# Kernel tuning notes

Hardware: AMD Instinct MI355X
Metric: run time of the kernel (lower is better)

Reference implementation:

```python
import jax, jax.numpy as jnp
import numpy as np


def gcn_conv(h, W, b, src, dst):
    # PyG GCNConv: h @ W, add self-loops, symmetric deg^-1/2 normalization,
    # scatter-add messages from src to dst, then add bias.
    n = h.shape[0]
    h = h @ W                                   # [N, out]
    loop = jnp.arange(n, dtype=src.dtype)
    row = jnp.concatenate([src, loop])          # message sources
    col = jnp.concatenate([dst, loop])          # aggregation targets
    deg = jax.ops.segment_sum(jnp.ones_like(col, dtype=h.dtype), col, num_segments=n)
    dinv = jnp.where(deg > 0, jax.lax.rsqrt(deg), 0.0)
    norm = dinv[row] * dinv[col]                # [E+N]
    out = jax.ops.segment_sum(h[row] * norm[:, None], col, num_segments=n)
    return out + b


def setup_inputs() -> dict:
    key = jax.random.key(0)
    ks = jax.random.split(key, 12)
    N, E = 50000, 800000
    in_dim, hid, out_dim = 768, 256, 128
    x = jax.random.normal(ks[0], (N, in_dim), dtype=jnp.float32)
    edge_index = jax.random.randint(ks[1], (2, E), 0, N, dtype=jnp.int64)

    def lin(k, fan_in, fan_out):
        bound = 1.0 / np.sqrt(fan_in)
        kw, kb = jax.random.split(k)
        W = jax.random.uniform(kw, (fan_in, fan_out), jnp.float32, -bound, bound)
        b = jax.random.uniform(kb, (fan_out,), jnp.float32, -bound, bound)
        return W, b

    W1, b1 = lin(ks[2], in_dim, hid)
    Wg1, bg1 = lin(ks[3], hid, hid)
    Wg2, bg2 = lin(ks[4], hid, hid)
    W2, b2 = lin(ks[5], hid, out_dim)
    Wc, bc = lin(ks[6], out_dim, 2)
    return {
        "x": x, "edge_index": edge_index,
        "W1": W1, "b1": b1, "Wg1": Wg1, "bg1": bg1,
        "Wg2": Wg2, "bg2": bg2, "W2": W2, "b2": b2,
        "Wc": Wc, "bc": bc, "batch_size": 1024,
    }


def reference(x, edge_index, W1, b1, Wg1, bg1, Wg2, bg2, W2, b2, Wc, bc, batch_size):
    src, dst = edge_index[0], edge_index[1]
    h = jax.nn.relu(x @ W1 + b1)                # linear_relu1
    h = gcn_conv(h, Wg1, bg1, src, dst)         # text1
    # dropout is identity in eval mode
    h = gcn_conv(h, Wg2, bg2, src, dst)         # text2
    h = jax.nn.relu(h @ W2 + b2)                # linear_relu2
    logits = h @ Wc + bc                        # classifier
    return logits[:batch_size]
```

## Files before the change

### kernel.cpp

```cpp
#include <hip/hip_runtime.h>
#include <hip/hip_bf16.h>
#include <cstdint>
#include <cstddef>
#include <type_traits>

typedef _Float16 half8 __attribute__((ext_vector_type(8)));
typedef _Float16 half4v __attribute__((ext_vector_type(4)));
typedef float float4v __attribute__((ext_vector_type(4)));


__global__ void k_zero_int(int* __restrict__ p, int n) {
  int i = blockIdx.x * blockDim.x + threadIdx.x;
  if (i < n) p[i] = 0;
}

__global__ void k_count(const int* __restrict__ dst, int* __restrict__ cnt, int E) {
  int e = blockIdx.x * blockDim.x + threadIdx.x;
  if (e < E) atomicAdd(&cnt[dst[e]], 1);
}

__global__ __launch_bounds__(1024) void k_scan_local(const int* __restrict__ cnt,
                                                     int* __restrict__ rowp,
                                                     int* __restrict__ bsum, int n) {
  __shared__ int sm[1024];
  int tid = threadIdx.x;
  int i = blockIdx.x * 1024 + tid;
  int v = (i < n) ? cnt[i] : 0;
  sm[tid] = v;
  __syncthreads();
  for (int off = 1; off < 1024; off <<= 1) {
    int t = (tid >= off) ? sm[tid - off] : 0;
    __syncthreads();
    sm[tid] += t;
    __syncthreads();
  }
  if (i < n) rowp[i] = sm[tid] - v;
  if (tid == 1023) bsum[blockIdx.x] = sm[1023];
}

__global__ __launch_bounds__(1024) void k_scan_sums(int* __restrict__ bsum, int nb) {
  __shared__ int sm[1024];
  int tid = threadIdx.x;
  int v = (tid < nb) ? bsum[tid] : 0;
  sm[tid] = v;
  __syncthreads();
  for (int off = 1; off < 1024; off <<= 1) {
    int t = (tid >= off) ? sm[tid - off] : 0;
    __syncthreads();
    sm[tid] += t;
    __syncthreads();
  }
  if (tid < nb) bsum[tid] = sm[tid] - v;
}

__global__ void k_finalize(int* __restrict__ rowp, const int* __restrict__ bsum,
                           const int* __restrict__ cnt, int* __restrict__ cursor,
                           float* __restrict__ dinv, int n, int E) {
  int i = blockIdx.x * blockDim.x + threadIdx.x;
  if (i < n) {
    int v = rowp[i] + bsum[i >> 10];
    rowp[i] = v;
    cursor[i] = v;
    dinv[i] = rsqrtf((float)(cnt[i] + 1));
  }
  if (i == 0) rowp[n] = E;
}

__global__ void k_fill(const int* __restrict__ src, const int* __restrict__ dst,
                       int* __restrict__ cursor, int* __restrict__ csr_src, int E) {
  int e = blockIdx.x * blockDim.x + threadIdx.x;
  if (e < E) {
    int pos = atomicAdd(&cursor[dst[e]], 1);
    csr_src[pos] = src[e];
  }
}


__global__ void k_w_convert_all(const float* __restrict__ W1, const float* __restrict__ Wg1,
                                const float* __restrict__ Wg2, _Float16* __restrict__ W1t,
                                _Float16* __restrict__ Wg1t, _Float16* __restrict__ Wg2t,
                                int in_dim, int hid) {
  int idx = blockIdx.x * blockDim.x + threadIdx.x;
  int n1 = in_dim * hid;
  int n2 = hid * hid;
  if (idx < n1) {
    int n = idx / in_dim, k = idx - n * in_dim;
    W1t[idx] = (_Float16)W1[(size_t)k * hid + n];
  } else if (idx < n1 + n2) {
    int i2 = idx - n1;
    int n = i2 / hid, k = i2 - n * hid;
    Wg1t[i2] = (_Float16)Wg1[(size_t)k * hid + n];
  } else if (idx < n1 + 2 * n2) {
    int i2 = idx - n1 - n2;
    int n = i2 / hid, k = i2 - n * hid;
    Wg2t[i2] = (_Float16)Wg2[(size_t)k * hid + n];
  }
}


#define LDSS 40

template <typename AT>
__device__ __forceinline__ half8 load_row_h8(const AT* __restrict__ p, bool ok) {
  half8 v = {};
  if (ok) {
    if constexpr (std::is_same_v<AT, float>) {
      float4 f0 = *(const float4*)p;
      float4 f1 = *(const float4*)(p + 4);
      v[0] = (_Float16)f0.x; v[1] = (_Float16)f0.y;
      v[2] = (_Float16)f0.z; v[3] = (_Float16)f0.w;
      v[4] = (_Float16)f1.x; v[5] = (_Float16)f1.y;
      v[6] = (_Float16)f1.z; v[7] = (_Float16)f1.w;
    } else {
      v = *(const half8*)p;
    }
  }
  return v;
}

template <typename AT, int RELU, int BIAS, int SCALE>
__global__ __launch_bounds__(256, 4) void k_gemm_mfma(const AT* __restrict__ A,
                                                      const _Float16* __restrict__ Bt,
                                                      const float* __restrict__ bias,
                                                      const float* __restrict__ rowscale,
                                                      _Float16* __restrict__ out,
                                                      int M, int N, int K) {
  __shared__ _Float16 Asm[2][64 * LDSS];
  __shared__ _Float16 Bsm[2][128 * LDSS];
  const int tid = threadIdx.x;
  const int bm = blockIdx.y * 64;
  const int bn = blockIdx.x * 128;
  const int wave = tid >> 6;
  const int wm = (wave >> 1) * 32;
  const int wn = (wave & 1) * 64;
  const int quad = (tid & 63) >> 4;
  const int l15 = tid & 15;

  const int ar = tid >> 2;
  const int ac = (tid & 3) * 8;
  const int br0 = tid >> 1;

  const int gra = bm + ar;
  const bool oka = gra < M;
  const AT* Apt = A + (size_t)gra * K + ac;
  const int br_0 = tid >> 2, bc_0 = (tid & 3) * 8;
  const int br_1 = (tid + 256) >> 2, bc_1 = ((tid + 256) & 3) * 8;
  const _Float16* Bp0 = Bt + (size_t)(bn + br_0) * K + bc_0;
  const _Float16* Bp1 = Bt + (size_t)(bn + br_1) * K + bc_1;

  _Float16* AsW = &Asm[0][0] + ar * LDSS + ac;
  _Float16* BsW0 = &Bsm[0][0] + br_0 * LDSS + bc_0;
  _Float16* BsW1 = &Bsm[0][0] + br_1 * LDSS + bc_1;
  const int abufstep = 64 * LDSS;
  const int bbufstep = 128 * LDSS;
  (void)br0;

  float4v acc[2][4];
#pragma unroll
  for (int i = 0; i < 2; ++i)
#pragma unroll
    for (int j = 0; j < 4; ++j) acc[i][j] = (float4v){0.f, 0.f, 0.f, 0.f};

  half8 pa = load_row_h8<AT>(Apt, oka);
  half8 pb0 = *(const half8*)Bp0;
  half8 pb1 = *(const half8*)Bp1;
  *(half8*)AsW = pa;
  *(half8*)BsW0 = pb0;
  *(half8*)BsW1 = pb1;

  const int nk = K >> 5;
  int buf = 0;
  for (int kt = 0; kt < nk; ++kt) {
    __syncthreads();
    if (kt + 1 < nk) {
      int k0 = (kt + 1) << 5;
      pa = load_row_h8<AT>(Apt + k0, oka);
      pb0 = *(const half8*)(Bp0 + k0);
      pb1 = *(const half8*)(Bp1 + k0);
    }
    const _Float16* Ab = &Asm[0][0] + buf * abufstep;
    const _Float16* Bb = &Bsm[0][0] + buf * bbufstep;
    half8 af[2], bf[4];
#pragma unroll
    for (int i = 0; i < 2; ++i)
      af[i] = *(const half8*)(Ab + (wm + i * 16 + l15) * LDSS + quad * 8);
#pragma unroll
    for (int j = 0; j < 4; ++j)
      bf[j] = *(const half8*)(Bb + (wn + j * 16 + l15) * LDSS + quad * 8);
#pragma unroll
    for (int i = 0; i < 2; ++i)
#pragma unroll
      for (int j = 0; j < 4; ++j)
        acc[i][j] = __builtin_amdgcn_mfma_f32_16x16x32_f16(af[i], bf[j], acc[i][j], 0, 0, 0);
    if (kt + 1 < nk) {
      int nbuf = buf ^ 1;
      *(half8*)(AsW + nbuf * abufstep) = pa;
      *(half8*)(BsW0 + nbuf * bbufstep) = pb0;
      *(half8*)(BsW1 + nbuf * bbufstep) = pb1;
    }
    buf ^= 1;
  }

#pragma unroll
  for (int j = 0; j < 4; ++j) {
    int c = bn + wn + j * 16 + l15;
    float bv = BIAS ? bias[c] : 0.f;
#pragma unroll
    for (int i = 0; i < 2; ++i) {
      int rbase = bm + wm + i * 16 + quad * 4;
      float4v a = acc[i][j];
#pragma unroll
      for (int reg = 0; reg < 4; ++reg) {
        int r = rbase + reg;
        if (r < M) {
          float v = a[reg] + bv;
          if (RELU) v = fmaxf(v, 0.f);
          if (SCALE) v *= rowscale[r];
          out[(size_t)r * N + c] = (_Float16)v;
        }
      }
    }
  }
}


template <int RELU, int BIAS>
__global__ __launch_bounds__(256) void k_gemm(const float* __restrict__ A,
                                              const float* __restrict__ B,
                                              const float* __restrict__ bias,
                                              float* __restrict__ C,
                                              int M, int N, int K) {
  __shared__ float As[16][68];
  __shared__ float Bs[16][68];
  const int bm = blockIdx.y * 64;
  const int bn = blockIdx.x * 64;
  const int tid = threadIdx.x;
  const int tr = (tid >> 4) << 2;
  const int tc = (tid & 15) << 2;
  const int lm  = tid >> 2;
  const int lk  = (tid & 3) << 2;
  const int lk2 = tid >> 4;
  const int ln  = (tid & 15) << 2;
  const bool arow_ok = (bm + lm) < M;
  const float* Aptr = A + (size_t)(bm + lm) * K + lk;
  const float* Bptr = B + (size_t)lk2 * N + bn + ln;
  float acc[4][4] = {};
  for (int k0 = 0; k0 < K; k0 += 16) {
    float4 a4 = make_float4(0.f, 0.f, 0.f, 0.f);
    if (arow_ok) a4 = *(const float4*)(Aptr + k0);
    float4 b4 = *(const float4*)(Bptr + (size_t)k0 * N);
    As[lk + 0][lm] = a4.x;
    As[lk + 1][lm] = a4.y;
    As[lk + 2][lm] = a4.z;
    As[lk + 3][lm] = a4.w;
    *(float4*)&Bs[lk2][ln] = b4;
    __syncthreads();
#pragma unroll
    for (int k = 0; k < 16; ++k) {
      float4 av = *(const float4*)&As[k][tr];
      float4 bv = *(const float4*)&Bs[k][tc];
      float a[4] = {av.x, av.y, av.z, av.w};
      float b[4] = {bv.x, bv.y, bv.z, bv.w};
#pragma unroll
      for (int i = 0; i < 4; ++i)
#pragma unroll
        for (int j = 0; j < 4; ++j) acc[i][j] += a[i] * b[j];
    }
    __syncthreads();
  }
  float bias_v[4] = {0.f, 0.f, 0.f, 0.f};
  if (BIAS) {
    float4 bb = *(const float4*)(bias + bn + tc);
    bias_v[0] = bb.x; bias_v[1] = bb.y; bias_v[2] = bb.z; bias_v[3] = bb.w;
  }
#pragma unroll
  for (int i = 0; i < 4; ++i) {
    int r = bm + tr + i;
    if (r < M) {
      float4 o;
      o.x = acc[i][0] + bias_v[0];
      o.y = acc[i][1] + bias_v[1];
      o.z = acc[i][2] + bias_v[2];
      o.w = acc[i][3] + bias_v[3];
      if (RELU) {
        o.x = fmaxf(o.x, 0.f); o.y = fmaxf(o.y, 0.f);
        o.z = fmaxf(o.z, 0.f); o.w = fmaxf(o.w, 0.f);
      }
      *(float4*)&C[(size_t)r * N + bn + tc] = o;
    }
  }
}


template <typename OT>
__global__ __launch_bounds__(256) void k_agg(const _Float16* __restrict__ t,
                                             const int* __restrict__ row_ptr,
                                             const int* __restrict__ csr_src,
                                             const float* __restrict__ dinv,
                                             const float* __restrict__ bias,
                                             OT* __restrict__ out, int n_nodes) {
  int w = (int)((blockIdx.x * 256 + threadIdx.x) >> 6);
  int lane = threadIdx.x & 63;
  if (w >= n_nodes) return;
  float di = dinv[w];
  half4v v = *(const half4v*)(t + (size_t)w * 256 + lane * 4);
  float ax = (float)v[0], ay = (float)v[1], az = (float)v[2], aw = (float)v[3];
  int e0 = row_ptr[w], e1 = row_ptr[w + 1];
  int e = e0;
  for (; e + 4 <= e1; e += 4) {
    int s0 = csr_src[e];
    int s1 = csr_src[e + 1];
    int s2 = csr_src[e + 2];
    int s3 = csr_src[e + 3];
    half4v u0 = *(const half4v*)(t + (size_t)s0 * 256 + lane * 4);
    half4v u1 = *(const half4v*)(t + (size_t)s1 * 256 + lane * 4);
    half4v u2 = *(const half4v*)(t + (size_t)s2 * 256 + lane * 4);
    half4v u3 = *(const half4v*)(t + (size_t)s3 * 256 + lane * 4);
    ax += (float)u0[0] + (float)u1[0] + (float)u2[0] + (float)u3[0];
    ay += (float)u0[1] + (float)u1[1] + (float)u2[1] + (float)u3[1];
    az += (float)u0[2] + (float)u1[2] + (float)u2[2] + (float)u3[2];
    aw += (float)u0[3] + (float)u1[3] + (float)u2[3] + (float)u3[3];
  }
  for (; e < e1; ++e) {
    int s = csr_src[e];
    half4v u = *(const half4v*)(t + (size_t)s * 256 + lane * 4);
    ax += (float)u[0]; ay += (float)u[1]; az += (float)u[2]; aw += (float)u[3];
  }
  const float4 b = ((const float4*)bias)[lane];
  if constexpr (std::is_same_v<OT, float>) {
    float4 o;
    o.x = ax * di + b.x; o.y = ay * di + b.y;
    o.z = az * di + b.z; o.w = aw * di + b.w;
    ((float4*)(out + (size_t)w * 256))[lane] = o;
  } else {
    half4v o;
    o[0] = (_Float16)(ax * di + b.x); o[1] = (_Float16)(ay * di + b.y);
    o[2] = (_Float16)(az * di + b.z); o[3] = (_Float16)(aw * di + b.w);
    *(half4v*)(out + (size_t)w * 256 + lane * 4) = o;
  }
}


__global__ __launch_bounds__(256) void k_cls(const float* __restrict__ h,
                                             const float* __restrict__ Wc,
                                             const float* __restrict__ bc,
                                             float* __restrict__ out, int M, int K) {
  __shared__ float w[512];
  for (int i = threadIdx.x; i < 2 * K; i += 256) w[i] = Wc[i];
  __syncthreads();
  int i = blockIdx.x * 256 + threadIdx.x;
  if (i >= M) return;
  float a0 = bc[0], a1 = bc[1];
  const float* hr = h + (size_t)i * K;
  for (int k = 0; k < K; ++k) {
    float a = hr[k];
    a0 += a * w[2 * k];
    a1 += a * w[2 * k + 1];
  }
  out[2 * i] = a0;
  out[2 * i + 1] = a1;
}


extern "C" void kernel_launch(void* const* d_in, const int* in_sizes, int n_in,
                              void* d_out, int out_size, void* d_ws, size_t ws_size,
                              hipStream_t stream) {
  const float* x   = (const float*)d_in[0];
  const int*   ei  = (const int*)d_in[1];
  const float* W1  = (const float*)d_in[2];
  const float* b1  = (const float*)d_in[3];
  const float* Wg1 = (const float*)d_in[4];
  const float* bg1 = (const float*)d_in[5];
  const float* Wg2 = (const float*)d_in[6];
  const float* bg2 = (const float*)d_in[7];
  const float* W2  = (const float*)d_in[8];
  const float* b2  = (const float*)d_in[9];
  const float* Wc  = (const float*)d_in[10];
  const float* bc  = (const float*)d_in[11];
  float* out = (float*)d_out;

  const int hid     = in_sizes[3];
  const int in_dim  = in_sizes[2] / hid;
  const int out_dim = in_sizes[9];
  const int N       = in_sizes[0] / in_dim;
  const int E       = in_sizes[1] / 2;
  const int Batch   = out_size / 2;

  const int* srcI = ei;
  const int* dstI = ei + E;

  char* ws = (char*)d_ws;
  size_t off = 0;
  auto alloc = [&](size_t bytes) -> void* {
    void* p = ws + off;
    off = (off + bytes + 255) & ~(size_t)255;
    return p;
  };
  _Float16* h0h  = (_Float16*)alloc((size_t)N * hid * 2);
  _Float16* t1h  = (_Float16*)alloc((size_t)N * hid * 2);
  _Float16* h1h  = (_Float16*)alloc((size_t)N * hid * 2);
  _Float16* t2h  = (_Float16*)alloc((size_t)N * hid * 2);
  _Float16* W1t  = (_Float16*)alloc((size_t)in_dim * hid * 2);
  _Float16* Wg1t = (_Float16*)alloc((size_t)hid * hid * 2);
  _Float16* Wg2t = (_Float16*)alloc((size_t)hid * hid * 2);
  float* agg2    = (float*)alloc((size_t)Batch * hid * 4);
  float* h3      = (float*)alloc((size_t)Batch * out_dim * 4);
  float* dinv    = (float*)alloc((size_t)N * 4);
  int*   cnt     = (int*)alloc((size_t)N * 4);
  int*   rowp    = (int*)alloc((size_t)(N + 1) * 4);
  int*   bsum    = (int*)alloc((size_t)1024 * 4);
  int*   cursor  = (int*)alloc((size_t)N * 4);
  int*   csrs    = (int*)alloc((size_t)E * 4);
  (void)ws_size; (void)n_in;

  dim3 blk(256);
  const int nb = (N + 1023) / 1024;

  k_zero_int<<<(N + 255) / 256, blk, 0, stream>>>(cnt, N);
  k_count<<<(E + 255) / 256, blk, 0, stream>>>(dstI, cnt, E);
  k_scan_local<<<nb, 1024, 0, stream>>>(cnt, rowp, bsum, N);
  k_scan_sums<<<1, 1024, 0, stream>>>(bsum, nb);
  k_finalize<<<(N + 255) / 256, blk, 0, stream>>>(rowp, bsum, cnt, cursor, dinv, N, E);
  k_fill<<<(E + 255) / 256, blk, 0, stream>>>(srcI, dstI, cursor, csrs, E);

  {
    int total = in_dim * hid + 2 * hid * hid;
    k_w_convert_all<<<(total + 255) / 256, blk, 0, stream>>>(W1, Wg1, Wg2, W1t, Wg1t, Wg2t, in_dim, hid);
  }

  dim3 gemm_grid(hid / 128, (N + 63) / 64);
  k_gemm_mfma<float, 1, 1, 0><<<gemm_grid, blk, 0, stream>>>(x, W1t, b1, nullptr, h0h, N, hid, in_dim);
  k_gemm_mfma<_Float16, 0, 0, 1><<<gemm_grid, blk, 0, stream>>>(h0h, Wg1t, nullptr, dinv, t1h, N, hid, hid);
  k_agg<_Float16><<<(N + 3) / 4, blk, 0, stream>>>(t1h, rowp, csrs, dinv, bg1, h1h, N);
  k_gemm_mfma<_Float16, 0, 0, 1><<<gemm_grid, blk, 0, stream>>>(h1h, Wg2t, nullptr, dinv, t2h, N, hid, hid);
  k_agg<float><<<(Batch + 3) / 4, blk, 0, stream>>>(t2h, rowp, csrs, dinv, bg2, agg2, Batch);
  k_gemm<1, 1><<<dim3(out_dim / 64, (Batch + 63) / 64), blk, 0, stream>>>(agg2, W2, b2, h3, Batch, out_dim, hid);
  k_cls<<<(Batch + 255) / 256, blk, 0, stream>>>(h3, Wc, bc, out, Batch, out_dim);
}
```

Baseline: 534.1 us.

## Use direct global-to-LDS loads, 128x128 tiles and XCD-aware block remap in MFMA GEMM

The MFMA GEMM now loads A and B tiles with global_load_lds, which writes straight into shared memory and skips the register round trip. For the fp32 first layer, A is staged in LDS as fp32 and converted to fp16 when fragments are read. The block tile grows from 64x128 to 128x128, giving each wave 4x4 MFMA accumulators and more reuse. Blocks are launched on a 1D grid and remapped so consecutive tiles land on the same XCD, which should improve L2 locality. In exchange, the padded LDS layout is dropped (possible bank conflicts), register pressure rises (launch bounds lowered to 3), fp32 A tiles double LDS use, and out-of-range rows are clamped rather than zeroed.

```diff
diff --git a/kernel.cpp b/kernel.cpp
--- a/kernel.cpp
+++ b/kernel.cpp
@@ -98,106 +98,125 @@
 }
 
 
-#define LDSS 40
-
-template <typename AT>
-__device__ __forceinline__ half8 load_row_h8(const AT* __restrict__ p, bool ok) {
-  half8 v = {};
-  if (ok) {
-    if constexpr (std::is_same_v<AT, float>) {
-      float4 f0 = *(const float4*)p;
-      float4 f1 = *(const float4*)(p + 4);
-      v[0] = (_Float16)f0.x; v[1] = (_Float16)f0.y;
-      v[2] = (_Float16)f0.z; v[3] = (_Float16)f0.w;
-      v[4] = (_Float16)f1.x; v[5] = (_Float16)f1.y;
-      v[6] = (_Float16)f1.z; v[7] = (_Float16)f1.w;
-    } else {
-      v = *(const half8*)p;
-    }
-  }
-  return v;
+__device__ __forceinline__ void gl_lds16(const void* g, void* l) {
+  __builtin_amdgcn_global_load_lds(
+      (const __attribute__((address_space(1))) void*)g,
+      (__attribute__((address_space(3))) void*)l, 16, 0, 0);
 }
 
 template <typename AT, int RELU, int BIAS, int SCALE>
-__global__ __launch_bounds__(256, 4) void k_gemm_mfma(const AT* __restrict__ A,
+__global__ __launch_bounds__(256, 3) void k_gemm_mfma(const AT* __restrict__ A,
                                                       const _Float16* __restrict__ Bt,
                                                       const float* __restrict__ bias,
                                                       const float* __restrict__ rowscale,
                                                       _Float16* __restrict__ out,
-                                                      int M, int N, int K) {
-  __shared__ _Float16 Asm[2][64 * LDSS];
-  __shared__ _Float16 Bsm[2][128 * LDSS];
+                                                      int M, int N, int K, int gx) {
+  __shared__ alignas(16) AT Asm[2][128 * 32];
+  __shared__ alignas(16) _Float16 Bsm[2][128 * 32];
+  constexpr int RA = (int)sizeof(AT);
+  constexpr int ABUFB = 128 * 32 * (int)sizeof(AT);
+  constexpr int BBUFB = 128 * 32 * 2;
+
   const int tid = threadIdx.x;
-  const int bm = blockIdx.y * 64;
-  const int bn = blockIdx.x * 128;
-  const int wave = tid >> 6;
-  const int wm = (wave >> 1) * 32;
-  const int wn = (wave & 1) * 64;
-  const int quad = (tid & 63) >> 4;
-  const int l15 = tid & 15;
-
-  const int ar = tid >> 2;
-  const int ac = (tid & 3) * 8;
-  const int br0 = tid >> 1;
-
-  const int gra = bm + ar;
-  const bool oka = gra < M;
-  const AT* Apt = A + (size_t)gra * K + ac;
-  const int br_0 = tid >> 2, bc_0 = (tid & 3) * 8;
-  const int br_1 = (tid + 256) >> 2, bc_1 = ((tid + 256) & 3) * 8;
-  const _Float16* Bp0 = Bt + (size_t)(bn + br_0) * K + bc_0;
-  const _Float16* Bp1 = Bt + (size_t)(bn + br_1) * K + bc_1;
-
-  _Float16* AsW = &Asm[0][0] + ar * LDSS + ac;
-  _Float16* BsW0 = &Bsm[0][0] + br_0 * LDSS + bc_0;
-  _Float16* BsW1 = &Bsm[0][0] + br_1 * LDSS + bc_1;
-  const int abufstep = 64 * LDSS;
-  const int bbufstep = 128 * LDSS;
-  (void)br0;
-
-  float4v acc[2][4];
-#pragma unroll
-  for (int i = 0; i < 2; ++i)
+  const int wv = tid >> 6;
+  const int ln = tid & 63;
+  const int quad = ln >> 4;
+  const int l15 = ln & 15;
+  const int wm = (wv >> 1) * 64;
+  const int wn = (wv & 1) * 64;
+
+  const int nwg = (int)gridDim.x;
+  const int orig = (int)blockIdx.x;
+  const int q = nwg >> 3, r = nwg & 7;
+  const int xcd = orig & 7, idx = orig >> 3;
+  const int wg = (xcd < r ? xcd * (q + 1) : r * (q + 1) + (xcd - r) * q) + idx;
+  const int bx = wg % gx;
+  const int by = wg / gx;
+  const int bm = by * 128;
+  const int bn = bx * 128;
+
+  const char* aSrcB[RA];
+  int aDstOff[RA];
+#pragma unroll
+  for (int rr = 0; rr < RA; ++rr) {
+    int p = rr * 4096 + wv * 1024 + ln * 16;
+    int row = p / (32 * (int)sizeof(AT));
+    int colB = p - row * 32 * (int)sizeof(AT);
+    int grow = bm + row; if (grow > M - 1) grow = M - 1;
+    aSrcB[rr] = (const char*)(A + (size_t)grow * K) + colB;
+    aDstOff[rr] = rr * 4096 + wv * 1024;
+  }
+  const char* bSrcB[2];
+  int bDstOff[2];
+#pragma unroll
+  for (int rr = 0; rr < 2; ++rr) {
+    int p = rr * 4096 + wv * 1024 + ln * 16;
+    int row = p >> 6;
+    int colB = p & 63;
+    bSrcB[rr] = (const char*)(Bt + (size_t)(bn + row) * K) + colB;
+    bDstOff[rr] = rr * 4096 + wv * 1024;
+  }
+
+  float4v acc[4][4];
+#pragma unroll
+  for (int i = 0; i < 4; ++i)
 #pragma unroll
     for (int j = 0; j < 4; ++j) acc[i][j] = (float4v){0.f, 0.f, 0.f, 0.f};
 
-  half8 pa = load_row_h8<AT>(Apt, oka);
-  half8 pb0 = *(const half8*)Bp0;
-  half8 pb1 = *(const half8*)Bp1;
-  *(half8*)AsW = pa;
-  *(half8*)BsW0 = pb0;
-  *(half8*)BsW1 = pb1;
-
   const int nk = K >> 5;
+
+  {
+    char* abase = (char*)&Asm[0][0];
+    char* bbase = (char*)&Bsm[0][0];
+#pragma unroll
+    for (int rr = 0; rr < RA; ++rr) gl_lds16(aSrcB[rr], abase + aDstOff[rr]);
+#pragma unroll
+    for (int rr = 0; rr < 2; ++rr) gl_lds16(bSrcB[rr], bbase + bDstOff[rr]);
+  }
+  __syncthreads();
+
   int buf = 0;
   for (int kt = 0; kt < nk; ++kt) {
-    __syncthreads();
     if (kt + 1 < nk) {
-      int k0 = (kt + 1) << 5;
-      pa = load_row_h8<AT>(Apt + k0, oka);
-      pb0 = *(const half8*)(Bp0 + k0);
-      pb1 = *(const half8*)(Bp1 + k0);
+      const size_t advA = (size_t)(kt + 1) * 32 * sizeof(AT);
+      const size_t advB = (size_t)(kt + 1) * 64;
+      char* abase = (char*)&Asm[0][0] + (buf ^ 1) * ABUFB;
+      char* bbase = (char*)&Bsm[0][0] + (buf ^ 1) * BBUFB;
+#pragma unroll
+      for (int rr = 0; rr < RA; ++rr) gl_lds16(aSrcB[rr] + advA, abase + aDstOff[rr]);
+#pragma unroll
+      for (int rr = 0; rr < 2; ++rr) gl_lds16(bSrcB[rr] + advB, bbase + bDstOff[rr]);
     }
-    const _Float16* Ab = &Asm[0][0] + buf * abufstep;
-    const _Float16* Bb = &Bsm[0][0] + buf * bbufstep;
-    half8 af[2], bf[4];
-#pragma unroll
-    for (int i = 0; i < 2; ++i)
-      af[i] = *(const half8*)(Ab + (wm + i * 16 + l15) * LDSS + quad * 8);
+
+    const AT* Ab = &Asm[buf][0];
+    const _Float16* Bb = &Bsm[buf][0];
+    half8 af[4], bf[4];
+#pragma unroll
+    for (int i = 0; i < 4; ++i) {
+      int rowa = wm + i * 16 + l15;
+      if constexpr (std::is_same_v<AT, float>) {
+        float4v f0 = *(const float4v*)(Ab + rowa * 32 + quad * 8);
+        float4v f1 = *(const float4v*)(Ab + rowa * 32 + quad * 8 + 4);
+        half8 h;
+        h[0] = (_Float16)f0[0]; h[1] = (_Float16)f0[1];
+        h[2] = (_Float16)f0[2]; h[3] = (_Float16)f0[3];
+        h[4] = (_Float16)f1[0]; h[5] = (_Float16)f1[1];
+        h[6] = (_Float16)f1[2]; h[7] = (_Float16)f1[3];
+        af[i] = h;
+      } else {
+        af[i] = *(const half8*)(Ab + rowa * 32 + quad * 8);
+      }
+    }
 #pragma unroll
     for (int j = 0; j < 4; ++j)
-      bf[j] = *(const half8*)(Bb + (wn + j * 16 + l15) * LDSS + quad * 8);
-#pragma unroll
-    for (int i = 0; i < 2; ++i)
+      bf[j] = *(const half8*)(Bb + (wn + j * 16 + l15) * 32 + quad * 8);
+#pragma unroll
+    for (int i = 0; i < 4; ++i)
 #pragma unroll
       for (int j = 0; j < 4; ++j)
         acc[i][j] = __builtin_amdgcn_mfma_f32_16x16x32_f16(af[i], bf[j], acc[i][j], 0, 0, 0);
-    if (kt + 1 < nk) {
-      int nbuf = buf ^ 1;
-      *(half8*)(AsW + nbuf * abufstep) = pa;
-      *(half8*)(BsW0 + nbuf * bbufstep) = pb0;
-      *(half8*)(BsW1 + nbuf * bbufstep) = pb1;
-    }
+
+    __syncthreads();
     buf ^= 1;
   }
 
@@ -206,17 +225,17 @@
     int c = bn + wn + j * 16 + l15;
     float bv = BIAS ? bias[c] : 0.f;
 #pragma unroll
-    for (int i = 0; i < 2; ++i) {
+    for (int i = 0; i < 4; ++i) {
       int rbase = bm + wm + i * 16 + quad * 4;
       float4v a = acc[i][j];
 #pragma unroll
       for (int reg = 0; reg < 4; ++reg) {
-        int r = rbase + reg;
-        if (r < M) {
+        int rr2 = rbase + reg;
+        if (rr2 < M) {
           float v = a[reg] + bv;
           if (RELU) v = fmaxf(v, 0.f);
-          if (SCALE) v *= rowscale[r];
-          out[(size_t)r * N + c] = (_Float16)v;
+          if (SCALE) v *= rowscale[rr2];
+          out[(size_t)rr2 * N + c] = (_Float16)v;
         }
       }
     }
@@ -428,11 +447,13 @@
     k_w_convert_all<<<(total + 255) / 256, blk, 0, stream>>>(W1, Wg1, Wg2, W1t, Wg1t, Wg2t, in_dim, hid);
   }
 
-  dim3 gemm_grid(hid / 128, (N + 63) / 64);
-  k_gemm_mfma<float, 1, 1, 0><<<gemm_grid, blk, 0, stream>>>(x, W1t, b1, nullptr, h0h, N, hid, in_dim);
-  k_gemm_mfma<_Float16, 0, 0, 1><<<gemm_grid, blk, 0, stream>>>(h0h, Wg1t, nullptr, dinv, t1h, N, hid, hid);
+  const int gx = hid / 128;
+  const int gy = (N + 127) / 128;
+  const int nwg = gx * gy;
+  k_gemm_mfma<float, 1, 1, 0><<<dim3(nwg), blk, 0, stream>>>(x, W1t, b1, nullptr, h0h, N, hid, in_dim, gx);
+  k_gemm_mfma<_Float16, 0, 0, 1><<<dim3(nwg), blk, 0, stream>>>(h0h, Wg1t, nullptr, dinv, t1h, N, hid, hid, gx);
   k_agg<_Float16><<<(N + 3) / 4, blk, 0, stream>>>(t1h, rowp, csrs, dinv, bg1, h1h, N);
-  k_gemm_mfma<_Float16, 0, 0, 1><<<gemm_grid, blk, 0, stream>>>(h1h, Wg2t, nullptr, dinv, t2h, N, hid, hid);
+  k_gemm_mfma<_Float16, 0, 0, 1><<<dim3(nwg), blk, 0, stream>>>(h1h, Wg2t, nullptr, dinv, t2h, N, hid, hid, gx);
   k_agg<float><<<(Batch + 3) / 4, blk, 0, stream>>>(t2h, rowp, csrs, dinv, bg2, agg2, Batch);
   k_gemm<1, 1><<<dim3(out_dim / 64, (Batch + 63) / 64), blk, 0, stream>>>(agg2, W2, b2, h3, Batch, out_dim, hid);
   k_cls<<<(Batch + 255) / 256, blk, 0, stream>>>(h3, Wc, bc, out, Batch, out_dim);
```

Measured after the change: 538.8 us. No clear change (+0.9%).
